# Kernel optimization log

Measured on AMD Instinct MI355X. Metric: run time of the kernel, lower is better.

## Reference

```python
import jax, jax.numpy as jnp
import numpy as np

N = 100000
E = 1600000
D = 64
NEG_SLOPE = 0.2


def setup_inputs() -> dict:
    key = jax.random.key(0)
    ks = jax.random.split(key, 16)
    inp = {}
    inp['x'] = jax.random.normal(ks[0], (N, D), dtype=jnp.float32)
    for i, name in enumerate(['edges_pos_out', 'edges_pos_in', 'edges_neg_out', 'edges_neg_in']):
        inp[name] = jax.random.randint(ks[1 + i], (2, E), 0, N, dtype=jnp.int64)
    s = 1.0 / np.sqrt(D)
    inp['gat_W'] = jax.random.normal(ks[5], (2, 4, D, D), dtype=jnp.float32) * s
    inp['gat_att_src'] = jax.random.normal(ks[6], (2, 4, D), dtype=jnp.float32) * s
    inp['gat_att_dst'] = jax.random.normal(ks[7], (2, 4, D), dtype=jnp.float32) * s
    inp['gat_bias'] = jnp.zeros((2, 4, D), dtype=jnp.float32)
    inp['mlp_W1'] = jax.random.normal(ks[8], (2, 5 * D, D), dtype=jnp.float32) * (1.0 / np.sqrt(5 * D))
    inp['mlp_b1'] = jnp.zeros((2, D), dtype=jnp.float32)
    inp['mlp_W2'] = jax.random.normal(ks[9], (2, D, D), dtype=jnp.float32) * s
    inp['mlp_b2'] = jnp.zeros((2, D), dtype=jnp.float32)
    return inp


def _gat(x, W, att_src, att_dst, bias, src, dst):
    # PyG GATConv, heads=1, add_self_loops=True
    n = x.shape[0]
    h = x @ W                                  # [N, D]
    a_src = h @ att_src                        # [N]
    a_dst = h @ att_dst                        # [N]
    loops = jnp.arange(n, dtype=src.dtype)
    s = jnp.concatenate([src, loops])
    d = jnp.concatenate([dst, loops])
    alpha = jax.nn.leaky_relu(a_src[s] + a_dst[d], NEG_SLOPE)   # [E+N]
    m = jax.ops.segment_max(alpha, d, num_segments=n)
    e = jnp.exp(alpha - m[d])
    z = jax.ops.segment_sum(e, d, num_segments=n)
    w = e / z[d]
    out = jax.ops.segment_sum(w[:, None] * h[s], d, num_segments=n)
    return out + bias


def _sdr_layer(x, edge_lists, W, a_s, a_d, b, W1, b1, W2, b2):
    feats = [x]
    for r, (src, dst) in enumerate(edge_lists):
        feats.append(_gat(x, W[r], a_s[r], a_d[r], b[r], src, dst))
    combined = jnp.concatenate(feats, axis=1)          # [N, 5D]
    hidden = jnp.tanh(combined @ W1 + b1)
    return hidden @ W2 + b2


def reference(x, edges_pos_out, edges_pos_in, edges_neg_out, edges_neg_in,
              gat_W, gat_att_src, gat_att_dst, gat_bias,
              mlp_W1, mlp_b1, mlp_W2, mlp_b2):
    edge_lists = [(e[0], e[1]) for e in
                  (edges_pos_out, edges_pos_in, edges_neg_out, edges_neg_in)]
    for l in range(gat_W.shape[0]):
        x = _sdr_layer(x, edge_lists, gat_W[l], gat_att_src[l], gat_att_dst[l],
                       gat_bias[l], mlp_W1[l], mlp_b1[l], mlp_W2[l], mlp_b2[l])
    return x
```

## Files before the change

kernel.cpp:

```cpp
#include <hip/hip_runtime.h>
#include <hip/hip_bf16.h>
#include <math.h>

#define D 64
#define NEG 0.2f
#define WPB 4
#define BLK 256
#define DPB 128
#define MAXNB 1024
#define CHUNK 16384
#define PCHUNK 8192

typedef __attribute__((ext_vector_type(8))) short bf8;
typedef __attribute__((ext_vector_type(4))) float f4;
typedef __attribute__((ext_vector_type(4))) int i4;

__device__ __forceinline__ float lrelu(float v) { return v > 0.f ? v : NEG * v; }

__device__ __forceinline__ unsigned short f2bf(float f) {
    unsigned u = __float_as_uint(f);
    u = (u + 0x7fffu + ((u >> 16) & 1u)) >> 16;
    return (unsigned short)u;
}
__device__ __forceinline__ bf8 ld_frag_g(const unsigned short* p) {
    i4 v = *(const i4*)p;
    return __builtin_bit_cast(bf8, v);
}

__device__ __forceinline__ const int* edge_ptr(const int* e0, const int* e1,
                                               const int* e2, const int* e3, int r)
{
    return (r == 0) ? e0 : (r == 1) ? e1 : (r == 2) ? e2 : e3;
}


__global__ __launch_bounds__(256) void k_bcount(
    const int* __restrict__ e0, const int* __restrict__ e1,
    const int* __restrict__ e2, const int* __restrict__ e3,
    int* __restrict__ bcnt, int E, int NB)
{
    int r = blockIdx.y;
    const int* dst = edge_ptr(e0, e1, e2, e3, r) + E;
    __shared__ int hist[MAXNB];
    for (int i = threadIdx.x; i < NB; i += 256) hist[i] = 0;
    __syncthreads();
    int base = blockIdx.x * CHUNK;
    int end = base + CHUNK < E ? base + CHUNK : E;
    for (int i = base + threadIdx.x; i < end; i += 256)
        atomicAdd(&hist[dst[i] >> 7], 1);
    __syncthreads();
    for (int i = threadIdx.x; i < NB; i += 256)
        if (hist[i]) atomicAdd(&bcnt[r * NB + i], hist[i]);
}

__global__ __launch_bounds__(1024) void k_bscan(
    const int* __restrict__ bcnt, int* __restrict__ boff,
    int* __restrict__ bcur, int* __restrict__ prefix, int E, int N, int NB)
{
    int r = blockIdx.y;
    __shared__ int sh[1024];
    int t = threadIdx.x;
    int v = (t < NB) ? bcnt[r * NB + t] : 0;
    sh[t] = v;
    __syncthreads();
    for (int off = 1; off < 1024; off <<= 1) {
        int add = (t >= off) ? sh[t - off] : 0;
        __syncthreads();
        sh[t] += add;
        __syncthreads();
    }
    if (t < NB) {
        int excl = sh[t] - v;
        boff[r * (NB + 1) + t] = excl;
        bcur[r * NB + t] = excl;
    }
    if (t == 0) {
        boff[r * (NB + 1) + NB] = E;
        prefix[(size_t)r * (N + 1) + N] = E;
    }
}

__global__ __launch_bounds__(256) void k_part(
    const int* __restrict__ e0, const int* __restrict__ e1,
    const int* __restrict__ e2, const int* __restrict__ e3,
    int* __restrict__ gcur, unsigned* __restrict__ staging, int E, int NB)
{
    __shared__ unsigned vals[PCHUNK];
    __shared__ unsigned short bkt[PCHUNK];
    __shared__ int hist[MAXNB];
    __shared__ int sbase[MAXNB];
    __shared__ int gdelta[MAXNB];
    __shared__ int ssum[256];
    int r = blockIdx.y;
    const int* ep = edge_ptr(e0, e1, e2, e3, r);
    const int* srcp = ep;
    const int* dstp = ep + E;
    int t = threadIdx.x;
    for (int j = t; j < MAXNB; j += 256) hist[j] = 0;
    __syncthreads();
    int begin = blockIdx.x * PCHUNK;
    int end = begin + PCHUNK < E ? begin + PCHUNK : E;
    int cnt = end - begin;
    for (int i = begin + t; i < end; i += 256)
        atomicAdd(&hist[dstp[i] >> 7], 1);
    __syncthreads();
    int h0 = hist[t * 4], h1 = hist[t * 4 + 1], h2 = hist[t * 4 + 2], h3 = hist[t * 4 + 3];
    int lsum = h0 + h1 + h2 + h3;
    ssum[t] = lsum;
    __syncthreads();
    for (int off = 1; off < 256; off <<= 1) {
        int a = (t >= off) ? ssum[t - off] : 0;
        __syncthreads();
        ssum[t] += a;
        __syncthreads();
    }
    int ex = ssum[t] - lsum;
    sbase[t * 4] = ex;
    sbase[t * 4 + 1] = ex + h0;
    sbase[t * 4 + 2] = ex + h0 + h1;
    sbase[t * 4 + 3] = ex + h0 + h1 + h2;
    __syncthreads();
    for (int j = t; j < NB; j += 256) {
        int c = hist[j];
        int gb = c ? atomicAdd(&gcur[r * NB + j], c) : 0;
        gdelta[j] = gb - sbase[j];
    }
    __syncthreads();
    for (int j = t; j < MAXNB; j += 256) hist[j] = 0;
    __syncthreads();
    for (int i = begin + t; i < end; i += 256) {
        int d = dstp[i];
        int s = srcp[i];
        int b = d >> 7;
        int rank = atomicAdd(&hist[b], 1);
        int p = sbase[b] + rank;
        vals[p] = ((unsigned)s << 7) | (unsigned)(d & 127);
        bkt[p] = (unsigned short)b;
    }
    __syncthreads();
    unsigned* stg = staging + (size_t)r * E;
    for (int p = t; p < cnt; p += 256)
        stg[p + gdelta[bkt[p]]] = vals[p];
}

__global__ __launch_bounds__(256) void k_place(
    const unsigned* __restrict__ staging, const int* __restrict__ boff,
    int* __restrict__ prefix, int* __restrict__ srcs, int N, int E, int NB)
{
    int r = blockIdx.y;
    int b = blockIdx.x;
    int t = threadIdx.x;
    __shared__ int lcount[DPB];
    __shared__ int ls[DPB];
    __shared__ int lcur[DPB];
    int gbase = boff[r * (NB + 1) + b];
    int bcnt = boff[r * (NB + 1) + b + 1] - gbase;
    if (t < DPB) lcount[t] = 0;
    __syncthreads();
    const unsigned* st = staging + (size_t)r * E + gbase;
    for (int i = t; i < bcnt; i += 256)
        atomicAdd(&lcount[st[i] & 127], 1);
    __syncthreads();
    if (t < DPB) ls[t] = lcount[t];
    __syncthreads();
    for (int off = 1; off < DPB; off <<= 1) {
        int add = (t < DPB && t >= off) ? ls[t - off] : 0;
        __syncthreads();
        if (t < DPB) ls[t] += add;
        __syncthreads();
    }
    int lo = b * DPB;
    if (t < DPB) {
        int excl = ls[t] - lcount[t];
        lcur[t] = excl;
        int d = lo + t;
        if (d < N) prefix[(size_t)r * (N + 1) + d] = gbase + excl;
    }
    __syncthreads();
    for (int i = t; i < bcnt; i += 256) {
        unsigned v = st[i];
        int pos = atomicAdd(&lcur[v & 127], 1);
        srcs[(size_t)r * E + gbase + pos] = (int)(v >> 7);
    }
}


__global__ __launch_bounds__(256) void k_xcast(
    const float* __restrict__ x, unsigned short* __restrict__ xb, int n4)
{
    int i = blockIdx.x * 256 + threadIdx.x;
    if (i < n4) {
        float4 v = ((const float4*)x)[i];
        ushort4 o;
        o.x = f2bf(v.x); o.y = f2bf(v.y); o.z = f2bf(v.z); o.w = f2bf(v.w);
        ((ushort4*)xb)[i] = o;
    }
}

__global__ __launch_bounds__(64) void k_pack(
    const float* __restrict__ gatW, const float* __restrict__ atS,
    const float* __restrict__ atD, const float* __restrict__ W1,
    const float* __restrict__ W2, unsigned short* __restrict__ WgP,
    unsigned short* __restrict__ W1P, unsigned short* __restrict__ W2P)
{
    int f = blockIdx.x;
    int L = threadIdx.x;
    int kg = L >> 4, c = L & 15;
    unsigned short vals[8];
    unsigned short* dst;
    if (f < 80) {
        int m = f / 10, rem = f % 10;
        int l = m / 4, r = m % 4;
        int kc = rem / 5, ct = rem % 5;
        const float* W = gatW + (size_t)(l * 4 + r) * D * D;
        if (ct < 4) {
#pragma unroll
            for (int j = 0; j < 8; j++) {
                int k = kc * 32 + kg * 8 + j;
                vals[j] = f2bf(W[k * D + ct * 16 + c]);
            }
        } else {
            const float* att = (c == 0) ? atS + (size_t)(l * 4 + r) * D
                                        : atD + (size_t)(l * 4 + r) * D;
#pragma unroll
            for (int j = 0; j < 8; j++) {
                int k = kc * 32 + kg * 8 + j;
                float s = 0.f;
                if (c < 2)
                    for (int cc = 0; cc < D; cc++) s += W[k * D + cc] * att[cc];
                vals[j] = f2bf(s);
            }
        }
        dst = WgP + ((size_t)f * 64 + L) * 8;
    } else if (f < 160) {
        int f2 = f - 80;
        int l = f2 / 40, rem = f2 % 40;
        int kc = rem / 4, ct = rem % 4;
        const float* W = W1 + (size_t)l * 5 * D * D;
#pragma unroll
        for (int j = 0; j < 8; j++) {
            int k = kc * 32 + kg * 8 + j;
            vals[j] = f2bf(W[k * D + ct * 16 + c]);
        }
        dst = W1P + ((size_t)f2 * 64 + L) * 8;
    } else {
        int f3 = f - 160;
        int l = f3 / 8, rem = f3 % 8;
        int kc = rem / 4, ct = rem % 4;
        const float* W = W2 + (size_t)l * D * D;
#pragma unroll
        for (int j = 0; j < 8; j++) {
            int k = kc * 32 + kg * 8 + j;
            vals[j] = f2bf(W[k * D + ct * 16 + c]);
        }
        dst = W2P + ((size_t)f3 * 64 + L) * 8;
    }
    i4 v = __builtin_bit_cast(i4, *(bf8*)vals);
    *(i4*)dst = v;
}


__device__ __forceinline__ void gemm_h_body(
    bf8 a0, bf8 a1, const unsigned short* __restrict__ WgPl,
    unsigned short* __restrict__ h, float* __restrict__ a_s,
    float* __restrict__ a_d, int n0, int kg, int lo, int L, int N)
{
#pragma unroll
    for (int r = 0; r < 4; r++) {
        const unsigned short* Wbase = WgPl + (size_t)r * 10 * 512;
#pragma unroll
        for (int ct = 0; ct < 5; ct++) {
            f4 acc = {0.f, 0.f, 0.f, 0.f};
            bf8 b0 = ld_frag_g(Wbase + (size_t)ct * 512 + (size_t)L * 8);
            bf8 b1 = ld_frag_g(Wbase + (size_t)(5 + ct) * 512 + (size_t)L * 8);
            acc = __builtin_amdgcn_mfma_f32_16x16x32_bf16(a0, b0, acc, 0, 0, 0);
            acc = __builtin_amdgcn_mfma_f32_16x16x32_bf16(a1, b1, acc, 0, 0, 0);
#pragma unroll
            for (int q = 0; q < 4; q++) {
                int node = n0 + kg * 4 + q;
                if (node < N) {
                    if (ct < 4)
                        h[((size_t)r * N + node) * D + ct * 16 + lo] = f2bf(acc[q]);
                    else if (lo == 0)
                        a_s[(size_t)r * N + node] = acc[q];
                    else if (lo == 1)
                        a_d[(size_t)r * N + node] = acc[q];
                }
            }
        }
    }
}

__global__ __launch_bounds__(BLK) void k_gemm_h(
    const unsigned short* __restrict__ xb, const unsigned short* __restrict__ WgPl,
    unsigned short* __restrict__ h, float* __restrict__ a_s,
    float* __restrict__ a_d, int N)
{
    int w = threadIdx.x >> 6, L = threadIdx.x & 63;
    int n0 = blockIdx.x * 64 + w * 16;
    int lo = L & 15, kg = L >> 4;
    int nA = n0 + lo; if (nA >= N) nA = N - 1;
    bf8 a0 = ld_frag_g(xb + (size_t)nA * D + kg * 8);
    bf8 a1 = ld_frag_g(xb + (size_t)nA * D + 32 + kg * 8);
    gemm_h_body(a0, a1, WgPl, h, a_s, a_d, n0, kg, lo, L, N);
}

__global__ __launch_bounds__(BLK) void k_agg(
    const unsigned short* __restrict__ h, const float* __restrict__ a_sall,
    const float* __restrict__ a_dall, const int* __restrict__ prefix,
    const int* __restrict__ srcsall, const float* __restrict__ gatB,
    unsigned short* __restrict__ g, int N, int E)
{
    __shared__ int2 pairs[WPB][64];
    int r = blockIdx.y;
    int w = threadIdx.x >> 6, lane = threadIdx.x & 63;
    int half = lane >> 5, fl = lane & 31;
    int d = (blockIdx.x * WPB + w) * 2 + half;
    if (d >= N) d = N - 1;

    const unsigned short* hr = h + (size_t)r * N * D;
    const float* a_src = a_sall + (size_t)r * N;
    const int* starts = prefix + (size_t)r * (N + 1);
    const int* srcs = srcsall + (size_t)r * E;

    int base = starts[d];
    int cnt = starts[d + 1] - base;
    float ad = a_dall[(size_t)r * N + d];

    float e_self = __expf(lrelu(a_src[d] + ad));
    float zpart = (fl == 0) ? e_self : 0.f;
    float accx, accy;
    {
        unsigned u = ((const unsigned*)(hr + (size_t)d * D))[fl];
        accx = e_self * __uint_as_float(u << 16);
        accy = e_self * __uint_as_float(u & 0xffff0000u);
    }

    int cntmax = max(cnt, __shfl_xor(cnt, 32));
    for (int c0 = 0; c0 < cntmax; c0 += 32) {
        int jj = c0 + fl;
        bool valid = jj < cnt;
        int s = valid ? srcs[base + jj] : 0;
        float e = valid ? __expf(lrelu(a_src[s] + ad)) : 0.f;
        zpart += e;
        pairs[w][lane] = make_int2(s * (int)(D * 2), __float_as_int(e));
        __threadfence_block();
        int lim = cntmax - c0; if (lim > 32) lim = 32;
        int rlim = (lim + 7) & ~7;
#pragma unroll 4
        for (int t = 0; t < rlim; t += 2) {
            i4 pv = *(const i4*)(&pairs[w][half * 32 + t]);
            unsigned uA = *(const unsigned*)((const char*)hr + pv.x + fl * 4);
            unsigned uB = *(const unsigned*)((const char*)hr + pv.z + fl * 4);
            float eA = __int_as_float(pv.y), eB = __int_as_float(pv.w);
            accx = fmaf(eA, __uint_as_float(uA << 16), accx);
            accy = fmaf(eA, __uint_as_float(uA & 0xffff0000u), accy);
            accx = fmaf(eB, __uint_as_float(uB << 16), accx);
            accy = fmaf(eB, __uint_as_float(uB & 0xffff0000u), accy);
        }
        __threadfence_block();
    }

    float z = zpart;
#pragma unroll
    for (int off = 16; off; off >>= 1) z += __shfl_xor(z, off);

    float rz = 1.f / z;
    float vlo = accx * rz + gatB[r * D + 2 * fl];
    float vhi = accy * rz + gatB[r * D + 2 * fl + 1];
    unsigned o = (unsigned)f2bf(vlo) | ((unsigned)f2bf(vhi) << 16);
    ((unsigned*)g)[((size_t)r * N + d) * 32 + fl] = o;
}

__global__ __launch_bounds__(BLK) void k_mlp(
    const unsigned short* __restrict__ xb, const unsigned short* __restrict__ g,
    const unsigned short* __restrict__ W1Pl, const float* __restrict__ b1l,
    const unsigned short* __restrict__ W2Pl, const float* __restrict__ b2l,
    void* __restrict__ outp, int N, int last,
    const unsigned short* __restrict__ WgPn, unsigned short* __restrict__ hn,
    float* __restrict__ a_sn, float* __restrict__ a_dn)
{
    __shared__ unsigned short sh[WPB][16 * 80];
    int w = threadIdx.x >> 6, L = threadIdx.x & 63;
    int n0 = blockIdx.x * 64 + w * 16;
    int lo = L & 15, kg = L >> 4;
    int nA = n0 + lo; if (nA >= N) nA = N - 1;

    f4 acc[4];
#pragma unroll
    for (int ct = 0; ct < 4; ct++) acc[ct] = (f4){0.f, 0.f, 0.f, 0.f};

#pragma unroll
    for (int p = 0; p < 5; p++) {
        const unsigned short* plane = (p == 0) ? xb : g + (size_t)(p - 1) * N * D;
#pragma unroll
        for (int kc2 = 0; kc2 < 2; kc2++) {
            bf8 a = ld_frag_g(plane + (size_t)nA * D + kc2 * 32 + kg * 8);
            int kc = p * 2 + kc2;
#pragma unroll
            for (int ct = 0; ct < 4; ct++) {
                bf8 b = ld_frag_g(W1Pl + ((size_t)(kc * 4 + ct) * 512 + (size_t)L * 8));
                acc[ct] = __builtin_amdgcn_mfma_f32_16x16x32_bf16(a, b, acc[ct], 0, 0, 0);
            }
        }
    }

    unsigned short* tile = &sh[w][0];
#pragma unroll
    for (int ct = 0; ct < 4; ct++) {
        float bb = b1l[ct * 16 + lo];
#pragma unroll
        for (int q = 0; q < 4; q++)
            tile[(kg * 4 + q) * 80 + ct * 16 + lo] = f2bf(tanhf(acc[ct][q] + bb));
    }
    __syncthreads();

    f4 o[4];
#pragma unroll
    for (int ct = 0; ct < 4; ct++) o[ct] = (f4){0.f, 0.f, 0.f, 0.f};
#pragma unroll
    for (int kc = 0; kc < 2; kc++) {
        const unsigned short* ap = tile + lo * 80 + kc * 32 + kg * 8;
        i4 av = *(const i4*)ap;
        bf8 a = __builtin_bit_cast(bf8, av);
#pragma unroll
        for (int ct = 0; ct < 4; ct++) {
            bf8 b = ld_frag_g(W2Pl + ((size_t)(kc * 4 + ct) * 512 + (size_t)L * 8));
            o[ct] = __builtin_amdgcn_mfma_f32_16x16x32_bf16(a, b, o[ct], 0, 0, 0);
        }
    }
    __syncthreads();
#pragma unroll
    for (int ct = 0; ct < 4; ct++) {
        float bb = b2l[ct * 16 + lo];
#pragma unroll
        for (int q = 0; q < 4; q++) {
            int node = n0 + kg * 4 + q;
            int col = ct * 16 + lo;
            float v = o[ct][q] + bb;
            if (node < N) {
                if (last) ((float*)outp)[(size_t)node * D + col] = v;
                else ((unsigned short*)outp)[(size_t)node * D + col] = f2bf(v);
            }
            if (!last) tile[(kg * 4 + q) * 80 + col] = f2bf(v);
        }
    }
    if (last) return;

    __syncthreads();
    bf8 a0, a1;
    {
        i4 v0 = *(const i4*)(tile + lo * 80 + kg * 8);
        i4 v1 = *(const i4*)(tile + lo * 80 + 32 + kg * 8);
        a0 = __builtin_bit_cast(bf8, v0);
        a1 = __builtin_bit_cast(bf8, v1);
    }
    gemm_h_body(a0, a1, WgPn, hn, a_sn, a_dn, n0, kg, lo, L, N);
}


extern "C" void kernel_launch(void* const* d_in, const int* in_sizes, int n_in,
                              void* d_out, int out_size, void* d_ws, size_t ws_size,
                              hipStream_t stream)
{
    const float* x    = (const float*)d_in[0];
    const int*   e0   = (const int*)d_in[1];
    const int*   e1   = (const int*)d_in[2];
    const int*   e2   = (const int*)d_in[3];
    const int*   e3   = (const int*)d_in[4];
    const float* gatW = (const float*)d_in[5];
    const float* atS  = (const float*)d_in[6];
    const float* atD  = (const float*)d_in[7];
    const float* gatB = (const float*)d_in[8];
    const float* W1   = (const float*)d_in[9];
    const float* b1   = (const float*)d_in[10];
    const float* W2   = (const float*)d_in[11];
    const float* b2   = (const float*)d_in[12];
    float* out = (float*)d_out;

    const int N = in_sizes[0] / D;
    const int E = in_sizes[1] / 2;
    const int NB = (N + DPB - 1) / DPB;

    size_t off = 0;
    auto alloc = [&](size_t bytes) { size_t o = off; off = (off + bytes + 255) & ~(size_t)255; return o; };
    unsigned short* xb    = (unsigned short*)((char*)d_ws + alloc((size_t)N * D * 2));
    unsigned short* xnext = (unsigned short*)((char*)d_ws + alloc((size_t)N * D * 2));
    unsigned short* h     = (unsigned short*)((char*)d_ws + alloc((size_t)4 * N * D * 2));
    unsigned short* g     = (unsigned short*)((char*)d_ws + alloc((size_t)4 * N * D * 2));
    unsigned* staging = (unsigned*)g;
    float* a_s   = (float*)((char*)d_ws + alloc((size_t)4 * N * 4));
    float* a_d   = (float*)((char*)d_ws + alloc((size_t)4 * N * 4));
    int* prefix  = (int*)((char*)d_ws + alloc((size_t)4 * (N + 1) * 4));
    int* srcs    = (int*)((char*)d_ws + alloc((size_t)4 * E * 4));
    int* bcnt    = (int*)((char*)d_ws + alloc((size_t)4 * NB * 4));
    int* boff    = (int*)((char*)d_ws + alloc((size_t)4 * (NB + 1) * 4));
    int* bcur    = (int*)((char*)d_ws + alloc((size_t)4 * NB * 4));
    unsigned short* WgP = (unsigned short*)((char*)d_ws + alloc((size_t)80 * 512 * 2));
    unsigned short* W1P = (unsigned short*)((char*)d_ws + alloc((size_t)80 * 512 * 2));
    unsigned short* W2P = (unsigned short*)((char*)d_ws + alloc((size_t)16 * 512 * 2));
    (void)ws_size;

    const int cntBlocks  = (E + CHUNK - 1) / CHUNK;
    const int partBlocks = (E + PCHUNK - 1) / PCHUNK;
    const int tileBlocks = (N + 63) / 64;
    const int aggBlocks  = (N + 7) / 8;

    k_pack<<<176, 64, 0, stream>>>(gatW, atS, atD, W1, W2, WgP, W1P, W2P);
    k_xcast<<<(N * D / 4 + 255) / 256, 256, 0, stream>>>(x, xb, N * D / 4);

    hipMemsetAsync(bcnt, 0, (size_t)4 * NB * 4, stream);
    k_bcount<<<dim3(cntBlocks, 4), 256, 0, stream>>>(e0, e1, e2, e3, bcnt, E, NB);
    k_bscan<<<dim3(1, 4), 1024, 0, stream>>>(bcnt, boff, bcur, prefix, E, N, NB);
    k_part<<<dim3(partBlocks, 4), 256, 0, stream>>>(e0, e1, e2, e3, bcur, staging, E, NB);
    k_place<<<dim3(NB, 4), 256, 0, stream>>>(staging, boff, prefix, srcs, N, E, NB);

    k_gemm_h<<<tileBlocks, BLK, 0, stream>>>(xb, WgP, h, a_s, a_d, N);
    k_agg<<<dim3(aggBlocks, 4), BLK, 0, stream>>>(
        h, a_s, a_d, prefix, srcs, gatB, g, N, E);
    k_mlp<<<tileBlocks, BLK, 0, stream>>>(
        xb, g, W1P, b1, W2P, b2, xnext, N, 0,
        WgP + (size_t)40 * 512, h, a_s, a_d);

    k_agg<<<dim3(aggBlocks, 4), BLK, 0, stream>>>(
        h, a_s, a_d, prefix, srcs, gatB + (size_t)4 * D, g, N, E);
    k_mlp<<<tileBlocks, BLK, 0, stream>>>(
        xnext, g, W1P + (size_t)40 * 512, b1 + D, W2P + (size_t)8 * 512, b2 + D,
        out, N, 1, nullptr, nullptr, nullptr, nullptr);
}
```

Measured before the change: 595.6 us.

## Sort destination nodes by in-degree to balance aggregation warps

Adds three kernels that build a counting-sort permutation of destination nodes by in-degree for each relation. The aggregation kernel then visits nodes in that order, so the two half-warps sharing a wavefront handle similar edge counts and lose less time to divergence. The inner loop rounds its trip count to pairs instead of groups of eight, cutting wasted padded iterations. In exchange it adds extra launches, an indirection load per node, and scattered output and self-row accesses that lose locality.

```diff
diff --git a/kernel.cpp b/kernel.cpp
--- a/kernel.cpp
+++ b/kernel.cpp
@@ -10,6 +10,7 @@
 #define MAXNB 1024
 #define CHUNK 16384
 #define PCHUNK 8192
+#define DB 256
 
 typedef __attribute__((ext_vector_type(8))) short bf8;
 typedef __attribute__((ext_vector_type(4))) float f4;
@@ -181,6 +182,75 @@
         unsigned v = st[i];
         int pos = atomicAdd(&lcur[v & 127], 1);
         srcs[(size_t)r * E + gbase + pos] = (int)(v >> 7);
+    }
+}
+
+
+__global__ __launch_bounds__(256) void k_dcount(
+    const int* __restrict__ prefix, int* __restrict__ dh, int N)
+{
+    int r = blockIdx.y;
+    __shared__ int hist[DB];
+    int t = threadIdx.x;
+    hist[t] = 0;
+    __syncthreads();
+    const int* st = prefix + (size_t)r * (N + 1);
+    int i0 = blockIdx.x * 2048;
+    int end = i0 + 2048 < N ? i0 + 2048 : N;
+    for (int i = i0 + t; i < end; i += 256) {
+        int deg = st[i + 1] - st[i];
+        int b = deg < DB ? deg : DB - 1;
+        atomicAdd(&hist[b], 1);
+    }
+    __syncthreads();
+    if (hist[t]) atomicAdd(&dh[r * DB + t], hist[t]);
+}
+
+__global__ __launch_bounds__(256) void k_dscan(
+    const int* __restrict__ dh, int* __restrict__ dcur)
+{
+    int r = blockIdx.y;
+    __shared__ int sh[DB];
+    int t = threadIdx.x;
+    int v = dh[r * DB + t];
+    sh[t] = v;
+    __syncthreads();
+    for (int off = 1; off < DB; off <<= 1) {
+        int add = (t >= off) ? sh[t - off] : 0;
+        __syncthreads();
+        sh[t] += add;
+        __syncthreads();
+    }
+    dcur[r * DB + t] = sh[t] - v;
+}
+
+__global__ __launch_bounds__(256) void k_dscat(
+    const int* __restrict__ prefix, int* __restrict__ dcur,
+    int* __restrict__ perm, int N)
+{
+    int r = blockIdx.y;
+    __shared__ int hist[DB];
+    __shared__ int rbase[DB];
+    int t = threadIdx.x;
+    hist[t] = 0;
+    __syncthreads();
+    const int* st = prefix + (size_t)r * (N + 1);
+    int i0 = blockIdx.x * 2048;
+    int end = i0 + 2048 < N ? i0 + 2048 : N;
+    for (int i = i0 + t; i < end; i += 256) {
+        int deg = st[i + 1] - st[i];
+        int b = deg < DB ? deg : DB - 1;
+        atomicAdd(&hist[b], 1);
+    }
+    __syncthreads();
+    rbase[t] = hist[t] ? atomicAdd(&dcur[r * DB + t], hist[t]) : 0;
+    hist[t] = 0;
+    __syncthreads();
+    for (int i = i0 + t; i < end; i += 256) {
+        int deg = st[i + 1] - st[i];
+        int b = deg < DB ? deg : DB - 1;
+        int rank = atomicAdd(&hist[b], 1);
+        perm[(size_t)r * N + rbase[b] + rank] = i;
     }
 }
 
@@ -308,15 +378,17 @@
 __global__ __launch_bounds__(BLK) void k_agg(
     const unsigned short* __restrict__ h, const float* __restrict__ a_sall,
     const float* __restrict__ a_dall, const int* __restrict__ prefix,
-    const int* __restrict__ srcsall, const float* __restrict__ gatB,
+    const int* __restrict__ srcsall, const int* __restrict__ perm,
+    const float* __restrict__ gatB,
     unsigned short* __restrict__ g, int N, int E)
 {
     __shared__ int2 pairs[WPB][64];
     int r = blockIdx.y;
     int w = threadIdx.x >> 6, lane = threadIdx.x & 63;
     int half = lane >> 5, fl = lane & 31;
-    int d = (blockIdx.x * WPB + w) * 2 + half;
-    if (d >= N) d = N - 1;
+    int idx = (blockIdx.x * WPB + w) * 2 + half;
+    if (idx >= N) idx = N - 1;
+    int d = perm[(size_t)r * N + idx];
 
     const unsigned short* hr = h + (size_t)r * N * D;
     const float* a_src = a_sall + (size_t)r * N;
@@ -346,8 +418,8 @@
         pairs[w][lane] = make_int2(s * (int)(D * 2), __float_as_int(e));
         __threadfence_block();
         int lim = cntmax - c0; if (lim > 32) lim = 32;
-        int rlim = (lim + 7) & ~7;
-#pragma unroll 4
+        int rlim = (lim + 1) & ~1;
+#pragma unroll 2
         for (int t = 0; t < rlim; t += 2) {
             i4 pv = *(const i4*)(&pairs[w][half * 32 + t]);
             unsigned uA = *(const unsigned*)((const char*)hr + pv.x + fl * 4);
@@ -496,6 +568,9 @@
     int* bcnt    = (int*)((char*)d_ws + alloc((size_t)4 * NB * 4));
     int* boff    = (int*)((char*)d_ws + alloc((size_t)4 * (NB + 1) * 4));
     int* bcur    = (int*)((char*)d_ws + alloc((size_t)4 * NB * 4));
+    int* perm    = (int*)((char*)d_ws + alloc((size_t)4 * N * 4));
+    int* dh      = (int*)((char*)d_ws + alloc((size_t)4 * DB * 4));
+    int* dcur    = (int*)((char*)d_ws + alloc((size_t)4 * DB * 4));
     unsigned short* WgP = (unsigned short*)((char*)d_ws + alloc((size_t)80 * 512 * 2));
     unsigned short* W1P = (unsigned short*)((char*)d_ws + alloc((size_t)80 * 512 * 2));
     unsigned short* W2P = (unsigned short*)((char*)d_ws + alloc((size_t)16 * 512 * 2));
@@ -505,25 +580,31 @@
     const int partBlocks = (E + PCHUNK - 1) / PCHUNK;
     const int tileBlocks = (N + 63) / 64;
     const int aggBlocks  = (N + 7) / 8;
+    const int dBlocks    = (N + 2047) / 2048;
 
     k_pack<<<176, 64, 0, stream>>>(gatW, atS, atD, W1, W2, WgP, W1P, W2P);
     k_xcast<<<(N * D / 4 + 255) / 256, 256, 0, stream>>>(x, xb, N * D / 4);
 
     hipMemsetAsync(bcnt, 0, (size_t)4 * NB * 4, stream);
+    hipMemsetAsync(dh, 0, (size_t)4 * DB * 4, stream);
     k_bcount<<<dim3(cntBlocks, 4), 256, 0, stream>>>(e0, e1, e2, e3, bcnt, E, NB);
     k_bscan<<<dim3(1, 4), 1024, 0, stream>>>(bcnt, boff, bcur, prefix, E, N, NB);
     k_part<<<dim3(partBlocks, 4), 256, 0, stream>>>(e0, e1, e2, e3, bcur, staging, E, NB);
     k_place<<<dim3(NB, 4), 256, 0, stream>>>(staging, boff, prefix, srcs, N, E, NB);
 
+    k_dcount<<<dim3(dBlocks, 4), 256, 0, stream>>>(prefix, dh, N);
+    k_dscan<<<dim3(1, 4), 256, 0, stream>>>(dh, dcur);
+    k_dscat<<<dim3(dBlocks, 4), 256, 0, stream>>>(prefix, dcur, perm, N);
+
     k_gemm_h<<<tileBlocks, BLK, 0, stream>>>(xb, WgP, h, a_s, a_d, N);
     k_agg<<<dim3(aggBlocks, 4), BLK, 0, stream>>>(
-        h, a_s, a_d, prefix, srcs, gatB, g, N, E);
+        h, a_s, a_d, prefix, srcs, perm, gatB, g, N, E);
     k_mlp<<<tileBlocks, BLK, 0, stream>>>(
         xb, g, W1P, b1, W2P, b2, xnext, N, 0,
         WgP + (size_t)40 * 512, h, a_s, a_d);
 
     k_agg<<<dim3(aggBlocks, 4), BLK, 0, stream>>>(
-        h, a_s, a_d, prefix, srcs, gatB + (size_t)4 * D, g, N, E);
+        h, a_s, a_d, prefix, srcs, perm, gatB + (size_t)4 * D, g, N, E);
     k_mlp<<<tileBlocks, BLK, 0, stream>>>(
         xnext, g, W1P + (size_t)40 * 512, b1 + D, W2P + (size_t)8 * 512, b2 + D,
         out, N, 1, nullptr, nullptr, nullptr, nullptr);
```

Result: slower. 637.5 us (+7.0%).

## Sort destination nodes by degree within windows to balance aggregation wavefronts

Applied to the files above, without the earlier changes.

Adds a kernel that bitonic-sorts each window of 256 destination nodes by in-degree and writes a permutation, which the aggregation kernel uses to choose which destination each half-wave processes. Pairing nodes of similar degree in the same wave cuts the divergence where one half waits on the longer neighbour list (cntmax). The inner gather loop padding also drops from multiples of 8 to multiples of 2, which removes wasted padded iterations. The costs are an extra kernel launch, one extra indirection per node, and less locality when writing g rows.

```diff
diff --git a/kernel.cpp b/kernel.cpp
--- a/kernel.cpp
+++ b/kernel.cpp
@@ -185,6 +185,40 @@
 }
 
 
+__global__ __launch_bounds__(256) void k_dwin(
+    const int* __restrict__ prefix, int* __restrict__ perm, int N)
+{
+    int r = blockIdx.y;
+    int t = threadIdx.x;
+    int i0 = blockIdx.x * 256;
+    const int* st = prefix + (size_t)r * (N + 1);
+    if (i0 + 256 > N) {
+        int i = i0 + t;
+        if (i < N) perm[(size_t)r * N + i] = i;
+        return;
+    }
+    __shared__ unsigned sh[256];
+    int i = i0 + t;
+    unsigned deg = (unsigned)(st[i + 1] - st[i]);
+    sh[t] = (deg << 8) | (unsigned)t;
+    __syncthreads();
+#pragma unroll
+    for (int k = 2; k <= 256; k <<= 1) {
+#pragma unroll
+        for (int j = k >> 1; j > 0; j >>= 1) {
+            int p = t ^ j;
+            unsigned a = sh[t], b = sh[p];
+            __syncthreads();
+            bool up = ((t & k) == 0);
+            unsigned lo = a < b ? a : b, hi = a < b ? b : a;
+            sh[t] = ((p > t) == up) ? lo : hi;
+            __syncthreads();
+        }
+    }
+    perm[(size_t)r * N + i0 + t] = i0 + (int)(sh[t] & 255u);
+}
+
+
 __global__ __launch_bounds__(256) void k_xcast(
     const float* __restrict__ x, unsigned short* __restrict__ xb, int n4)
 {
@@ -308,15 +342,17 @@
 __global__ __launch_bounds__(BLK) void k_agg(
     const unsigned short* __restrict__ h, const float* __restrict__ a_sall,
     const float* __restrict__ a_dall, const int* __restrict__ prefix,
-    const int* __restrict__ srcsall, const float* __restrict__ gatB,
+    const int* __restrict__ srcsall, const int* __restrict__ perm,
+    const float* __restrict__ gatB,
     unsigned short* __restrict__ g, int N, int E)
 {
     __shared__ int2 pairs[WPB][64];
     int r = blockIdx.y;
     int w = threadIdx.x >> 6, lane = threadIdx.x & 63;
     int half = lane >> 5, fl = lane & 31;
-    int d = (blockIdx.x * WPB + w) * 2 + half;
-    if (d >= N) d = N - 1;
+    int idx = (blockIdx.x * WPB + w) * 2 + half;
+    if (idx >= N) idx = N - 1;
+    int d = perm[(size_t)r * N + idx];
 
     const unsigned short* hr = h + (size_t)r * N * D;
     const float* a_src = a_sall + (size_t)r * N;
@@ -346,8 +382,8 @@
         pairs[w][lane] = make_int2(s * (int)(D * 2), __float_as_int(e));
         __threadfence_block();
         int lim = cntmax - c0; if (lim > 32) lim = 32;
-        int rlim = (lim + 7) & ~7;
-#pragma unroll 4
+        int rlim = (lim + 1) & ~1;
+#pragma unroll 2
         for (int t = 0; t < rlim; t += 2) {
             i4 pv = *(const i4*)(&pairs[w][half * 32 + t]);
             unsigned uA = *(const unsigned*)((const char*)hr + pv.x + fl * 4);
@@ -496,6 +532,7 @@
     int* bcnt    = (int*)((char*)d_ws + alloc((size_t)4 * NB * 4));
     int* boff    = (int*)((char*)d_ws + alloc((size_t)4 * (NB + 1) * 4));
     int* bcur    = (int*)((char*)d_ws + alloc((size_t)4 * NB * 4));
+    int* perm    = (int*)((char*)d_ws + alloc((size_t)4 * N * 4));
     unsigned short* WgP = (unsigned short*)((char*)d_ws + alloc((size_t)80 * 512 * 2));
     unsigned short* W1P = (unsigned short*)((char*)d_ws + alloc((size_t)80 * 512 * 2));
     unsigned short* W2P = (unsigned short*)((char*)d_ws + alloc((size_t)16 * 512 * 2));
@@ -505,6 +542,7 @@
     const int partBlocks = (E + PCHUNK - 1) / PCHUNK;
     const int tileBlocks = (N + 63) / 64;
     const int aggBlocks  = (N + 7) / 8;
+    const int winBlocks  = (N + 255) / 256;
 
     k_pack<<<176, 64, 0, stream>>>(gatW, atS, atD, W1, W2, WgP, W1P, W2P);
     k_xcast<<<(N * D / 4 + 255) / 256, 256, 0, stream>>>(x, xb, N * D / 4);
@@ -515,15 +553,17 @@
     k_part<<<dim3(partBlocks, 4), 256, 0, stream>>>(e0, e1, e2, e3, bcur, staging, E, NB);
     k_place<<<dim3(NB, 4), 256, 0, stream>>>(staging, boff, prefix, srcs, N, E, NB);
 
+    k_dwin<<<dim3(winBlocks, 4), 256, 0, stream>>>(prefix, perm, N);
+
     k_gemm_h<<<tileBlocks, BLK, 0, stream>>>(xb, WgP, h, a_s, a_d, N);
     k_agg<<<dim3(aggBlocks, 4), BLK, 0, stream>>>(
-        h, a_s, a_d, prefix, srcs, gatB, g, N, E);
+        h, a_s, a_d, prefix, srcs, perm, gatB, g, N, E);
     k_mlp<<<tileBlocks, BLK, 0, stream>>>(
         xb, g, W1P, b1, W2P, b2, xnext, N, 0,
         WgP + (size_t)40 * 512, h, a_s, a_d);
 
     k_agg<<<dim3(aggBlocks, 4), BLK, 0, stream>>>(
-        h, a_s, a_d, prefix, srcs, gatB + (size_t)4 * D, g, N, E);
+        h, a_s, a_d, prefix, srcs, perm, gatB + (size_t)4 * D, g, N, E);
     k_mlp<<<tileBlocks, BLK, 0, stream>>>(
         xnext, g, W1P + (size_t)40 * 512, b1 + D, W2P + (size_t)8 * 512, b2 + D,
         out, N, 1, nullptr, nullptr, nullptr, nullptr);
```

New measurement: 655.3 us. 10.0% more time.
